# Kernel optimization log

Hardware: AMD Instinct MI355X
Metric: run time of the kernel (lower is better)

Reference implementation:

```python
import jax, jax.numpy as jnp
import numpy as np

N_NODES = 50000
N_EDGES = 800000
IN_DIM, HID_DIM, N_CLASS = 128, 128, 2
DROPOUT_P = 0.5
NEG_SLOPE = 0.01  # F.leaky_relu default


def gcn_conv(x, src, dst, W, b, n_nodes):
    """PyG GCNConv: add self-loops, sym-normalize, aggregate, then bias."""
    loops = jnp.arange(n_nodes, dtype=src.dtype)
    s = jnp.concatenate([src, loops])
    d = jnp.concatenate([dst, loops])
    # degree on A + I (edge weights = 1), counted at destination
    deg = jax.ops.segment_sum(jnp.ones_like(d, dtype=x.dtype), d, num_segments=n_nodes)
    dis = jnp.where(deg > 0, jax.lax.rsqrt(deg), 0.0)  # deg^{-1/2}
    norm = dis[s] * dis[d]                               # [E+N]
    h = x @ W                                            # [N, out]
    msg = h[s] * norm[:, None]                           # gather + scale
    out = jax.ops.segment_sum(msg, d, num_segments=n_nodes)  # scatter-add
    return out + b


def dropout(x, p, key):
    keep = 1.0 - p
    mask = jax.random.bernoulli(key, keep, x.shape)
    return jnp.where(mask, x / keep, 0.0)


def setup_inputs() -> dict:
    key = jax.random.key(0)
    ks = jax.random.split(key, 8)
    x = jax.random.normal(ks[0], (N_NODES, IN_DIM), dtype=jnp.float32)
    edge_index = jax.random.randint(ks[1], (2, N_EDGES), 0, N_NODES, dtype=jnp.int64)
    def glorot(k, fin, fout):
        lim = np.sqrt(6.0 / (fin + fout)).astype(np.float32)
        return jax.random.uniform(k, (fin, fout), jnp.float32, -lim, lim)
    W1 = glorot(ks[2], IN_DIM, HID_DIM)
    W2 = glorot(ks[3], HID_DIM, HID_DIM)
    W3 = glorot(ks[4], HID_DIM, N_CLASS)
    b1 = jnp.zeros((HID_DIM,), jnp.float32)
    b2 = jnp.zeros((HID_DIM,), jnp.float32)
    b3 = jnp.zeros((N_CLASS,), jnp.float32)
    return {"x": x, "edge_index": edge_index, "W1": W1, "b1": b1,
            "W2": W2, "b2": b2, "W3": W3, "b3": b3}


def reference(x, edge_index, W1, b1, W2, b2, W3, b3):
    src, dst = edge_index[0], edge_index[1]
    n = x.shape[0]
    dkey = jax.random.key(42)
    k1, k2 = jax.random.split(dkey)
    h = gcn_conv(x, src, dst, W1, b1, n)
    h = jax.nn.leaky_relu(h, NEG_SLOPE)
    h = dropout(h, DROPOUT_P, k1)
    h = gcn_conv(h, src, dst, W2, b2, n)
    h = jax.nn.leaky_relu(h, NEG_SLOPE)
    h = dropout(h, DROPOUT_P, k2)
    h = gcn_conv(h, src, dst, W3, b3, n)
    return jax.nn.log_softmax(h, axis=1)
```

## Files before the change

kernel.cpp:

```cpp
#include <hip/hip_runtime.h>
#include <stdint.h>

#define N_NODES 50000
#define N_EDGES 800000
#define DIM     128
#define NB   196
#define CAP  8192
#define CHUNK 2048
#define NBLK 391
#define GNODES 16
#define GGRID 3125
#define GCAP 2048
#define G3NODES 128
#define G3CAP 4096
#define ZBLK 98

typedef __attribute__((ext_vector_type(8))) unsigned short ushort8_t;
typedef __attribute__((ext_vector_type(8))) short bfrag;
typedef __attribute__((ext_vector_type(4))) float f32x4;

__host__ __device__ inline void threefry2x32(uint32_t k0, uint32_t k1,
                                             uint32_t x0, uint32_t x1,
                                             uint32_t& o0, uint32_t& o1) {
    uint32_t ks0 = k0, ks1 = k1, ks2 = k0 ^ k1 ^ 0x1BD11BDAu;
    uint32_t v0 = x0 + ks0, v1 = x1 + ks1;
#define TF_R(r) { v0 += v1; v1 = (v1 << (r)) | (v1 >> (32 - (r))); v1 ^= v0; }
    TF_R(13) TF_R(15) TF_R(26) TF_R(6)
    v0 += ks1; v1 += ks2 + 1u;
    TF_R(17) TF_R(29) TF_R(16) TF_R(24)
    v0 += ks2; v1 += ks0 + 2u;
    TF_R(13) TF_R(15) TF_R(26) TF_R(6)
    v0 += ks0; v1 += ks1 + 3u;
    TF_R(17) TF_R(29) TF_R(16) TF_R(24)
    v0 += ks1; v1 += ks2 + 4u;
    TF_R(13) TF_R(15) TF_R(26) TF_R(6)
    v0 += ks2; v1 += ks0 + 5u;
#undef TF_R
    o0 = v0; o1 = v1;
}

__device__ inline float drop_scale(uint32_t kk0, uint32_t kk1, uint32_t i) {
    uint32_t b0, b1;
    threefry2x32(kk0, kk1, 0u, i, b0, b1);
    uint32_t bits = b0 ^ b1;
    return (bits >> 31) ? 0.0f : 2.0f;
}

__device__ inline float bf2f(ushort u) {
    return __uint_as_float(((uint32_t)u) << 16);
}
__device__ inline float bfpair_lo(uint32_t u) { return __uint_as_float(u << 16); }
__device__ inline float bfpair_hi(uint32_t u) { return __uint_as_float(u & 0xffff0000u); }

__device__ inline ushort f2bf_rne(float f) {
    uint32_t bits = __float_as_uint(f);
    uint32_t lsb = (bits >> 16) & 1u;
    bits += 0x7fffu + lsb;
    return (ushort)(bits >> 16);
}

__device__ inline void acc8(float* acc, uint4 u, float d) {
    acc[0] += d * bfpair_lo(u.x); acc[1] += d * bfpair_hi(u.x);
    acc[2] += d * bfpair_lo(u.y); acc[3] += d * bfpair_hi(u.y);
    acc[4] += d * bfpair_lo(u.z); acc[5] += d * bfpair_hi(u.z);
    acc[6] += d * bfpair_lo(u.w); acc[7] += d * bfpair_hi(u.w);
}
__device__ inline void acc8p(float* acc, uint4 u) {
    acc[0] += bfpair_lo(u.x); acc[1] += bfpair_hi(u.x);
    acc[2] += bfpair_lo(u.y); acc[3] += bfpair_hi(u.y);
    acc[4] += bfpair_lo(u.z); acc[5] += bfpair_hi(u.z);
    acc[6] += bfpair_lo(u.w); acc[7] += bfpair_hi(u.w);
}

template<int F32A, int SCALE>
__device__ inline void gemm_body(const ushort* __restrict__ Xb,
                                 const float* __restrict__ Xf,
                                 const ushort* __restrict__ Wt,
                                 const float* __restrict__ dis,
                                 ushort* __restrict__ Hb, int gb, int tid) {
    int w = tid >> 6, lane = tid & 63;
    int m0 = gb * 128 + w * 32;
    int lrow = lane & 15, quad = lane >> 4;
    f32x4 acc[2][8] = {};
    for (int kt = 0; kt < DIM; kt += 32) {
        bfrag a[2], b[8];
        #pragma unroll
        for (int t = 0; t < 2; ++t) {
            int m = m0 + t * 16 + lrow;
            if (m >= N_NODES) m = 0;
            if (F32A) {
                const float* p = Xf + (size_t)m * DIM + kt + quad * 8;
                f32x4 v0 = *(const f32x4*)p;
                f32x4 v1 = *(const f32x4*)(p + 4);
                #pragma unroll
                for (int j = 0; j < 4; ++j) {
                    a[t][j]     = (short)f2bf_rne(v0[j]);
                    a[t][j + 4] = (short)f2bf_rne(v1[j]);
                }
            } else {
                a[t] = *(const bfrag*)(Xb + (size_t)m * DIM + kt + quad * 8);
            }
        }
        #pragma unroll
        for (int c = 0; c < 8; ++c) {
            int n = c * 16 + lrow;
            b[c] = *(const bfrag*)(Wt + (size_t)n * DIM + kt + quad * 8);
        }
        #pragma unroll
        for (int t = 0; t < 2; ++t)
            #pragma unroll
            for (int c = 0; c < 8; ++c)
                acc[t][c] = __builtin_amdgcn_mfma_f32_16x16x32_bf16(a[t], b[c], acc[t][c], 0, 0, 0);
    }
    #pragma unroll
    for (int t = 0; t < 2; ++t) {
        #pragma unroll
        for (int r = 0; r < 4; ++r) {
            int rowi = m0 + t * 16 + quad * 4 + r;
            if (rowi < N_NODES) {
                float dv = SCALE ? dis[rowi] : 1.0f;
                #pragma unroll
                for (int c = 0; c < 8; ++c) {
                    int feat = c * 16 + lrow;
                    float z = SCALE ? acc[t][c][r] * dv : acc[t][c][r];
                    Hb[(size_t)rowi * DIM + feat] = f2bf_rne(z);
                }
            }
        }
    }
}

__global__ __launch_bounds__(256) void k_prep(const float* __restrict__ W1,
                                              const float* __restrict__ W2,
                                              ushort* __restrict__ W1t,
                                              ushort* __restrict__ W2t,
                                              const int* __restrict__ src,
                                              const int* __restrict__ dst,
                                              uint32_t* __restrict__ gcur,
                                              uint32_t* __restrict__ packed,
                                              float* __restrict__ h3s) {
    __shared__ uint32_t h[NB];
    int b = blockIdx.x;
    int t = threadIdx.x;
    if (b < NBLK) {
        uint32_t dc[CHUNK / 256], sc[CHUNK / 256];
        if (t < NB) h[t] = 0u;
        __syncthreads();
        int base = b * CHUNK;
        #pragma unroll
        for (int i = 0; i < CHUNK / 256; ++i) {
            int e = base + i * 256 + t;
            if (e < N_EDGES) {
                dc[i] = (uint32_t)dst[e];
                sc[i] = (uint32_t)src[e];
                atomicAdd(&h[dc[i] >> 8], 1u);
            } else {
                dc[i] = 0xffffffffu;
            }
        }
        __syncthreads();
        if (t < NB) {
            uint32_t c = h[t];
            h[t] = c ? atomicAdd(&gcur[t], c) : 0u;
        }
        __syncthreads();
        #pragma unroll
        for (int i = 0; i < CHUNK / 256; ++i) {
            if (dc[i] != 0xffffffffu) {
                uint32_t d = dc[i];
                uint32_t s = sc[i];
                uint32_t bk = d >> 8;
                uint32_t pos = atomicAdd(&h[bk], 1u);
                if (pos < CAP)
                    packed[(size_t)bk * CAP + pos] = ((d & 255u) << 16) | s;
            }
        }
    } else if (b < NBLK + 128) {
        int j = (b - NBLK) * 256 + t;
        const float* W = (j < DIM * DIM) ? W1 : W2;
        ushort* Wt = (j < DIM * DIM) ? W1t : W2t;
        int i = j & (DIM * DIM - 1);
        int k = i >> 7, n = i & 127;
        Wt[n * DIM + k] = f2bf_rne(W[k * DIM + n]);
    } else {
        int idx = (b - NBLK - 128) * 256 + t;
        if (idx < (N_NODES * 2) / 4) {
            f32x4 z = {0.f, 0.f, 0.f, 0.f};
            ((f32x4*)h3s)[idx] = z;
        }
    }
}

__global__ __launch_bounds__(256) void k_fill(const uint32_t* __restrict__ gcur,
                                              const uint32_t* __restrict__ packed,
                                              uint32_t* __restrict__ row,
                                              float* __restrict__ dis,
                                              ushort* __restrict__ col16,
                                              const float* __restrict__ x,
                                              const ushort* __restrict__ W1t,
                                              ushort* __restrict__ Hb) {
    __shared__ uint32_t sdeg[256];
    __shared__ uint32_t scan[256];
    __shared__ uint32_t cur[256];
    int b = blockIdx.x;
    int t = threadIdx.x;
    if (b >= NB) {
        gemm_body<1, 0>(nullptr, x, W1t, nullptr, Hb, b - NB, t);
        return;
    }
    uint32_t n = gcur[b];
    scan[t] = (t < b) ? gcur[t] : 0u;
    __syncthreads();
    for (int off = 1; off < 256; off <<= 1) {
        uint32_t xx = (t >= off) ? scan[t - off] : 0u;
        __syncthreads();
        scan[t] += xx;
        __syncthreads();
    }
    uint32_t cbase = scan[255];
    __syncthreads();
    uint32_t pbase = (uint32_t)b * CAP;
    sdeg[t] = 0u;
    __syncthreads();
    for (uint32_t i = t; i < n; i += 256) {
        uint32_t u = packed[pbase + i];
        atomicAdd(&sdeg[u >> 16], 1u);
    }
    __syncthreads();
    uint32_t myd = sdeg[t];
    scan[t] = myd;
    __syncthreads();
    for (int off = 1; off < 256; off <<= 1) {
        uint32_t xx = (t >= off) ? scan[t - off] : 0u;
        __syncthreads();
        scan[t] += xx;
        __syncthreads();
    }
    uint32_t excl = scan[t] - myd;
    cur[t] = excl;
    int v = b * 256 + t;
    if (v <= N_NODES) row[v] = cbase + excl;
    if (v < N_NODES)  dis[v] = 1.0f / sqrtf((float)(myd + 1u));
    __syncthreads();
    for (uint32_t i = t; i < n; i += 256) {
        uint32_t u = packed[pbase + i];
        uint32_t pos = cbase + atomicAdd(&cur[u >> 16], 1u);
        col16[pos] = (ushort)(u & 0xffffu);
    }
}

template<int CLS, int SRCDIS>
__global__ __launch_bounds__(256) void k_gather_t(const uint32_t* __restrict__ row,
                                                  const ushort* __restrict__ col16,
                                                  const float* __restrict__ dis,
                                                  const ushort* __restrict__ Hb,
                                                  const float* __restrict__ bias,
                                                  ushort* __restrict__ OUTb,
                                                  const float* __restrict__ W3,
                                                  float* __restrict__ h3s,
                                                  uint32_t kk0, uint32_t kk1) {
    __shared__ ushort scol[GCAP];
    __shared__ uint32_t srow[GNODES + 1];
    int tid = threadIdx.x;
    int nbase = blockIdx.x * GNODES;
    if (tid <= GNODES) srow[tid] = row[nbase + tid];
    __syncthreads();
    uint32_t eLo = srow[0];
    uint32_t count = srow[GNODES] - eLo;
    bool staged = count <= GCAP;
    if (staged) {
        for (uint32_t i = tid; i < count; i += 256) scol[i] = col16[eLo + i];
    }
    __syncthreads();

    int nl = tid >> 4;
    int q  = tid & 15;
    int v = nbase + nl;
    float dv = dis[v];
    float acc[8];
    {
        uint4 u = *(const uint4*)(Hb + (size_t)v * DIM + q * 8);
        acc[0] = bfpair_lo(u.x); acc[1] = bfpair_hi(u.x);
        acc[2] = bfpair_lo(u.y); acc[3] = bfpair_hi(u.y);
        acc[4] = bfpair_lo(u.z); acc[5] = bfpair_hi(u.z);
        acc[6] = bfpair_lo(u.w); acc[7] = bfpair_hi(u.w);
        if (SRCDIS) {
            #pragma unroll
            for (int j = 0; j < 8; ++j) acc[j] *= dv;
        }
    }

    uint32_t e0 = srow[nl] - eLo, e1 = srow[nl + 1] - eLo;
    uint32_t e = e0;
    if (staged) {
        for (; e + 8 <= e1; e += 8) {
            uint32_t s0 = scol[e],     s1 = scol[e + 1];
            uint32_t s2 = scol[e + 2], s3 = scol[e + 3];
            uint32_t s4 = scol[e + 4], s5 = scol[e + 5];
            uint32_t s6 = scol[e + 6], s7 = scol[e + 7];
            uint4 u0 = *(const uint4*)(Hb + (size_t)s0 * DIM + q * 8);
            uint4 u1 = *(const uint4*)(Hb + (size_t)s1 * DIM + q * 8);
            uint4 u2 = *(const uint4*)(Hb + (size_t)s2 * DIM + q * 8);
            uint4 u3 = *(const uint4*)(Hb + (size_t)s3 * DIM + q * 8);
            uint4 u4 = *(const uint4*)(Hb + (size_t)s4 * DIM + q * 8);
            uint4 u5 = *(const uint4*)(Hb + (size_t)s5 * DIM + q * 8);
            uint4 u6 = *(const uint4*)(Hb + (size_t)s6 * DIM + q * 8);
            uint4 u7 = *(const uint4*)(Hb + (size_t)s7 * DIM + q * 8);
            if (SRCDIS) {
                float d0 = dis[s0], d1 = dis[s1], d2 = dis[s2], d3 = dis[s3];
                float d4 = dis[s4], d5 = dis[s5], d6 = dis[s6], d7 = dis[s7];
                acc8(acc, u0, d0); acc8(acc, u1, d1);
                acc8(acc, u2, d2); acc8(acc, u3, d3);
                acc8(acc, u4, d4); acc8(acc, u5, d5);
                acc8(acc, u6, d6); acc8(acc, u7, d7);
            } else {
                acc8p(acc, u0); acc8p(acc, u1); acc8p(acc, u2); acc8p(acc, u3);
                acc8p(acc, u4); acc8p(acc, u5); acc8p(acc, u6); acc8p(acc, u7);
            }
        }
        for (; e + 4 <= e1; e += 4) {
            uint32_t s0 = scol[e],     s1 = scol[e + 1];
            uint32_t s2 = scol[e + 2], s3 = scol[e + 3];
            uint4 u0 = *(const uint4*)(Hb + (size_t)s0 * DIM + q * 8);
            uint4 u1 = *(const uint4*)(Hb + (size_t)s1 * DIM + q * 8);
            uint4 u2 = *(const uint4*)(Hb + (size_t)s2 * DIM + q * 8);
            uint4 u3 = *(const uint4*)(Hb + (size_t)s3 * DIM + q * 8);
            if (SRCDIS) {
                float d0 = dis[s0], d1 = dis[s1], d2 = dis[s2], d3 = dis[s3];
                acc8(acc, u0, d0); acc8(acc, u1, d1);
                acc8(acc, u2, d2); acc8(acc, u3, d3);
            } else {
                acc8p(acc, u0); acc8p(acc, u1); acc8p(acc, u2); acc8p(acc, u3);
            }
        }
        for (; e < e1; ++e) {
            uint32_t s0 = scol[e];
            uint4 u0 = *(const uint4*)(Hb + (size_t)s0 * DIM + q * 8);
            if (SRCDIS) acc8(acc, u0, dis[s0]);
            else        acc8p(acc, u0);
        }
    } else {
        for (; e < e1; ++e) {
            uint32_t s0 = col16[eLo + e];
            uint4 u0 = *(const uint4*)(Hb + (size_t)s0 * DIM + q * 8);
            if (SRCDIS) acc8(acc, u0, dis[s0]);
            else        acc8p(acc, u0);
        }
    }

    int cbase = q * 8;
    uint32_t ibase = (uint32_t)(v * DIM + cbase);
    if (CLS == 0) {
        ushort8_t o;
        #pragma unroll
        for (int j = 0; j < 8; ++j) {
            float z = acc[j] * dv + bias[cbase + j];
            z = (z >= 0.f) ? z : 0.01f * z;
            z *= drop_scale(kk0, kk1, ibase + j);
            o[j] = f2bf_rne(z);
        }
        *((ushort8_t*)(OUTb + (size_t)v * DIM + cbase)) = o;
    } else {
        float o0 = 0.f, o1 = 0.f;
        #pragma unroll
        for (int j = 0; j < 8; ++j) {
            float z = acc[j] * dv + bias[cbase + j];
            z = (z >= 0.f) ? z : 0.01f * z;
            z *= drop_scale(kk0, kk1, ibase + j);
            o0 += z * W3[(cbase + j) * 2 + 0];
            o1 += z * W3[(cbase + j) * 2 + 1];
        }
        o0 += __shfl_xor(o0, 1); o0 += __shfl_xor(o0, 2);
        o0 += __shfl_xor(o0, 4); o0 += __shfl_xor(o0, 8);
        o1 += __shfl_xor(o1, 1); o1 += __shfl_xor(o1, 2);
        o1 += __shfl_xor(o1, 4); o1 += __shfl_xor(o1, 8);
        if (q == 0) {
            atomicAdd(&h3s[v * 2 + 0], o0 * dv);
            atomicAdd(&h3s[v * 2 + 1], o1 * dv);
        }
    }
}

__global__ __launch_bounds__(256) void k_gemm_bf16(const ushort* __restrict__ Xb,
                                                   const ushort* __restrict__ Wt,
                                                   const float* __restrict__ dis,
                                                   ushort* __restrict__ Hb) {
    gemm_body<0, 1>(Xb, nullptr, Wt, dis, Hb, blockIdx.x, threadIdx.x);
}

__global__ __launch_bounds__(256) void k_gather3(const uint32_t* __restrict__ row,
                                                 const ushort* __restrict__ col16,
                                                 const float* __restrict__ dis,
                                                 const float* __restrict__ H3s,
                                                 const float* __restrict__ b3,
                                                 float* __restrict__ out) {
    __shared__ ushort scol[G3CAP];
    __shared__ uint32_t srow[G3NODES + 1];
    int tid = threadIdx.x;
    int nbase = blockIdx.x * G3NODES;
    int nend = nbase + G3NODES; if (nend > N_NODES) nend = N_NODES;
    int nloc = nend - nbase;
    for (int i = tid; i <= nloc; i += 256) srow[i] = row[nbase + i];
    __syncthreads();
    uint32_t eLo = srow[0];
    uint32_t count = srow[nloc] - eLo;
    bool staged = count <= G3CAP;
    if (staged) {
        for (uint32_t i = tid; i < count; i += 256) scol[i] = col16[eLo + i];
    }
    __syncthreads();

    int nl = tid >> 1;
    int par = tid & 1;
    int v = nbase + nl;
    if (v >= N_NODES) return;
    const float2* H2 = (const float2*)H3s;
    float z0 = 0.f, z1 = 0.f;
    if (par == 0) {
        float2 h = H2[v];
        z0 = h.x; z1 = h.y;
    }
    uint32_t e0 = srow[nl] - eLo, e1 = srow[nl + 1] - eLo;
    if (staged) {
        for (uint32_t e = e0 + par; e < e1; e += 2) {
            float2 ha = H2[scol[e]];
            z0 += ha.x; z1 += ha.y;
        }
    } else {
        for (uint32_t e = e0 + par; e < e1; e += 2) {
            float2 ha = H2[col16[eLo + e]];
            z0 += ha.x; z1 += ha.y;
        }
    }
    z0 += __shfl_xor(z0, 1);
    z1 += __shfl_xor(z1, 1);
    if (par) return;
    float dv = dis[v];
    z0 = z0 * dv + b3[0];
    z1 = z1 * dv + b3[1];
    float m = fmaxf(z0, z1);
    float lse = m + logf(expf(z0 - m) + expf(z1 - m));
    out[v * 2 + 0] = z0 - lse;
    out[v * 2 + 1] = z1 - lse;
}

extern "C" void kernel_launch(void* const* d_in, const int* in_sizes, int n_in,
                              void* d_out, int out_size, void* d_ws, size_t ws_size,
                              hipStream_t stream) {
    const float* x  = (const float*)d_in[0];
    const int*   ei = (const int*)d_in[1];
    const float* W1 = (const float*)d_in[2];
    const float* b1 = (const float*)d_in[3];
    const float* W2 = (const float*)d_in[4];
    const float* b2 = (const float*)d_in[5];
    const float* W3 = (const float*)d_in[6];
    const float* b3 = (const float*)d_in[7];
    float* out = (float*)d_out;

    const int* src = ei;
    const int* dst = ei + N_EDGES;

    uint32_t* wsu = (uint32_t*)d_ws;
    float*    wsf = (float*)d_ws;
    uint32_t* gcur   = wsu;
    uint32_t* row    = wsu + 256;
    float*    dis    = wsf + 50304;
    uint32_t* packed = wsu + 100352;
    ushort*   col16  = (ushort*)(wsu + 1705984);
    ushort*   Hb     = (ushort*)(wsu + 2106112);
    ushort*   Bb     = (ushort*)(wsu + 8506112);
    ushort*   W1t    = (ushort*)(wsu + 11706112);
    ushort*   W2t    = (ushort*)(wsu + 11714304);
    float*    h3s    = wsf + 11722496;

    uint32_t k1a, k1b, k2a, k2b;
    threefry2x32(0u, 42u, 0u, 0u, k1a, k1b);
    threefry2x32(0u, 42u, 0u, 1u, k2a, k2b);

    hipMemsetAsync(gcur, 0, 256 * sizeof(uint32_t), stream);

    k_prep<<<NBLK + 128 + ZBLK, 256, 0, stream>>>(W1, W2, W1t, W2t,
                                                  src, dst, gcur, packed, h3s);

    k_fill<<<NB + 391, 256, 0, stream>>>(gcur, packed, row, dis, col16,
                                         x, W1t, Hb);

    k_gather_t<0, 1><<<GGRID, 256, 0, stream>>>(row, col16, dis, Hb, b1, Bb,
                                                nullptr, nullptr, k1a, k1b);

    k_gemm_bf16<<<(N_NODES + 127) / 128, 256, 0, stream>>>(Bb, W2t, dis, Hb);
    k_gather_t<1, 0><<<GGRID, 256, 0, stream>>>(row, col16, dis, Hb, b2, nullptr,
                                                W3, h3s, k2a, k2b);

    k_gather3<<<(N_NODES + G3NODES - 1) / G3NODES, 256, 0, stream>>>(row, col16, dis,
                                                                     h3s, b3, out);
}
```

Measured before the change: 213.9 us.

## Fuse layer-1 gather with layer-2 MFMA GEMM in one kernel

Replaces the layer-1 gather kernel and the separate bf16 GEMM kernel with one fused kernel. Each 64-node block aggregates neighbours, applies bias, leaky-relu and dropout, writes the rows to a scratch buffer, then runs MFMA over those rows against W2 and writes the dis-scaled result. This removes one kernel launch and the global round trip between kernels. In exchange the grid is much smaller (782 blocks instead of 3125), so there is less parallelism to hide gather latency. The GEMM also re-reads its rows from global memory after a block-level barrier, which relies on the block's own writes being visible to it.

```diff
diff --git a/kernel.cpp b/kernel.cpp
--- a/kernel.cpp
+++ b/kernel.cpp
@@ -11,6 +11,9 @@
 #define GNODES 16
 #define GGRID 3125
 #define GCAP 2048
+#define FN   64
+#define FBLK 782
+#define GCAP_F 3072
 #define G3NODES 128
 #define G3CAP 4096
 #define ZBLK 98
@@ -249,16 +252,148 @@
     }
 }
 
-template<int CLS, int SRCDIS>
-__global__ __launch_bounds__(256) void k_gather_t(const uint32_t* __restrict__ row,
-                                                  const ushort* __restrict__ col16,
-                                                  const float* __restrict__ dis,
-                                                  const ushort* __restrict__ Hb,
-                                                  const float* __restrict__ bias,
-                                                  ushort* __restrict__ OUTb,
-                                                  const float* __restrict__ W3,
-                                                  float* __restrict__ h3s,
-                                                  uint32_t kk0, uint32_t kk1) {
+__global__ __launch_bounds__(256) void k_fused(const uint32_t* __restrict__ row,
+                                               const ushort* __restrict__ col16,
+                                               const float* __restrict__ dis,
+                                               const ushort* __restrict__ Hb,
+                                               const float* __restrict__ bias,
+                                               ushort* __restrict__ Bs,
+                                               const ushort* __restrict__ W2t,
+                                               ushort* __restrict__ Hb2,
+                                               uint32_t kk0, uint32_t kk1) {
+    __shared__ ushort scol[GCAP_F];
+    __shared__ uint32_t srow[FN + 1];
+    int tid = threadIdx.x;
+    int nbase = blockIdx.x * FN;
+    int top = N_NODES - nbase; if (top > FN) top = FN;
+    for (int i = tid; i <= top; i += 256) srow[i] = row[nbase + i];
+    __syncthreads();
+    uint32_t eLo = srow[0];
+    uint32_t count = srow[top] - eLo;
+    bool staged = count <= GCAP_F;
+    if (staged) {
+        for (uint32_t i = tid; i < count; i += 256) scol[i] = col16[eLo + i];
+    }
+    __syncthreads();
+
+    int nl = tid >> 4;
+    int q  = tid & 15;
+    #pragma unroll
+    for (int r = 0; r < 4; ++r) {
+        int lr = r * 16 + nl;
+        int v = nbase + lr;
+        if (lr < top) {
+            float dv = dis[v];
+            float acc[8];
+            {
+                uint4 u = *(const uint4*)(Hb + (size_t)v * DIM + q * 8);
+                acc[0] = bfpair_lo(u.x); acc[1] = bfpair_hi(u.x);
+                acc[2] = bfpair_lo(u.y); acc[3] = bfpair_hi(u.y);
+                acc[4] = bfpair_lo(u.z); acc[5] = bfpair_hi(u.z);
+                acc[6] = bfpair_lo(u.w); acc[7] = bfpair_hi(u.w);
+                #pragma unroll
+                for (int j = 0; j < 8; ++j) acc[j] *= dv;
+            }
+            uint32_t e0 = srow[lr] - eLo, e1 = srow[lr + 1] - eLo;
+            uint32_t e = e0;
+            if (staged) {
+                for (; e + 8 <= e1; e += 8) {
+                    uint32_t s0 = scol[e],     s1 = scol[e + 1];
+                    uint32_t s2 = scol[e + 2], s3 = scol[e + 3];
+                    uint32_t s4 = scol[e + 4], s5 = scol[e + 5];
+                    uint32_t s6 = scol[e + 6], s7 = scol[e + 7];
+                    uint4 u0 = *(const uint4*)(Hb + (size_t)s0 * DIM + q * 8);
+                    uint4 u1 = *(const uint4*)(Hb + (size_t)s1 * DIM + q * 8);
+                    uint4 u2 = *(const uint4*)(Hb + (size_t)s2 * DIM + q * 8);
+                    uint4 u3 = *(const uint4*)(Hb + (size_t)s3 * DIM + q * 8);
+                    uint4 u4 = *(const uint4*)(Hb + (size_t)s4 * DIM + q * 8);
+                    uint4 u5 = *(const uint4*)(Hb + (size_t)s5 * DIM + q * 8);
+                    uint4 u6 = *(const uint4*)(Hb + (size_t)s6 * DIM + q * 8);
+                    uint4 u7 = *(const uint4*)(Hb + (size_t)s7 * DIM + q * 8);
+                    float d0 = dis[s0], d1 = dis[s1], d2 = dis[s2], d3 = dis[s3];
+                    float d4 = dis[s4], d5 = dis[s5], d6 = dis[s6], d7 = dis[s7];
+                    acc8(acc, u0, d0); acc8(acc, u1, d1);
+                    acc8(acc, u2, d2); acc8(acc, u3, d3);
+                    acc8(acc, u4, d4); acc8(acc, u5, d5);
+                    acc8(acc, u6, d6); acc8(acc, u7, d7);
+                }
+                for (; e + 4 <= e1; e += 4) {
+                    uint32_t s0 = scol[e],     s1 = scol[e + 1];
+                    uint32_t s2 = scol[e + 2], s3 = scol[e + 3];
+                    uint4 u0 = *(const uint4*)(Hb + (size_t)s0 * DIM + q * 8);
+                    uint4 u1 = *(const uint4*)(Hb + (size_t)s1 * DIM + q * 8);
+                    uint4 u2 = *(const uint4*)(Hb + (size_t)s2 * DIM + q * 8);
+                    uint4 u3 = *(const uint4*)(Hb + (size_t)s3 * DIM + q * 8);
+                    float d0 = dis[s0], d1 = dis[s1], d2 = dis[s2], d3 = dis[s3];
+                    acc8(acc, u0, d0); acc8(acc, u1, d1);
+                    acc8(acc, u2, d2); acc8(acc, u3, d3);
+                }
+                for (; e < e1; ++e) {
+                    uint32_t s0 = scol[e];
+                    uint4 u0 = *(const uint4*)(Hb + (size_t)s0 * DIM + q * 8);
+                    acc8(acc, u0, dis[s0]);
+                }
+            } else {
+                for (; e < e1; ++e) {
+                    uint32_t s0 = col16[eLo + e];
+                    uint4 u0 = *(const uint4*)(Hb + (size_t)s0 * DIM + q * 8);
+                    acc8(acc, u0, dis[s0]);
+                }
+            }
+            int cbase = q * 8;
+            uint32_t ibase = (uint32_t)(v * DIM + cbase);
+            ushort8_t o;
+            #pragma unroll
+            for (int j = 0; j < 8; ++j) {
+                float z = acc[j] * dv + bias[cbase + j];
+                z = (z >= 0.f) ? z : 0.01f * z;
+                z *= drop_scale(kk0, kk1, ibase + j);
+                o[j] = f2bf_rne(z);
+            }
+            *((ushort8_t*)(Bs + (size_t)v * DIM + cbase)) = o;
+        }
+    }
+    __syncthreads();
+
+    int w = tid >> 6, lane = tid & 63;
+    int lrow = lane & 15, quad = lane >> 4;
+    int m = nbase + w * 16 + lrow;
+    const ushort* Arow = Bs + (size_t)m * DIM;
+    #pragma unroll
+    for (int half = 0; half < 2; ++half) {
+        f32x4 acc[4] = {};
+        for (int kt = 0; kt < DIM; kt += 32) {
+            bfrag a = *(const bfrag*)(Arow + kt + quad * 8);
+            #pragma unroll
+            for (int c = 0; c < 4; ++c) {
+                int n = (half * 4 + c) * 16 + lrow;
+                bfrag b = *(const bfrag*)(W2t + (size_t)n * DIM + kt + quad * 8);
+                acc[c] = __builtin_amdgcn_mfma_f32_16x16x32_bf16(a, b, acc[c], 0, 0, 0);
+            }
+        }
+        #pragma unroll
+        for (int rr = 0; rr < 4; ++rr) {
+            int rowi = nbase + w * 16 + quad * 4 + rr;
+            if (rowi < N_NODES) {
+                float dvv = dis[rowi];
+                #pragma unroll
+                for (int c = 0; c < 4; ++c) {
+                    int feat = (half * 4 + c) * 16 + lrow;
+                    Hb2[(size_t)rowi * DIM + feat] = f2bf_rne(acc[c][rr] * dvv);
+                }
+            }
+        }
+    }
+}
+
+__global__ __launch_bounds__(256) void k_gather2(const uint32_t* __restrict__ row,
+                                                 const ushort* __restrict__ col16,
+                                                 const float* __restrict__ dis,
+                                                 const ushort* __restrict__ Hb,
+                                                 const float* __restrict__ bias,
+                                                 const float* __restrict__ W3,
+                                                 float* __restrict__ h3s,
+                                                 uint32_t kk0, uint32_t kk1) {
     __shared__ ushort scol[GCAP];
     __shared__ uint32_t srow[GNODES + 1];
     int tid = threadIdx.x;
@@ -284,10 +419,6 @@
         acc[2] = bfpair_lo(u.y); acc[3] = bfpair_hi(u.y);
         acc[4] = bfpair_lo(u.z); acc[5] = bfpair_hi(u.z);
         acc[6] = bfpair_lo(u.w); acc[7] = bfpair_hi(u.w);
-        if (SRCDIS) {
-            #pragma unroll
-            for (int j = 0; j < 8; ++j) acc[j] *= dv;
-        }
     }
 
     uint32_t e0 = srow[nl] - eLo, e1 = srow[nl + 1] - eLo;
@@ -306,17 +437,8 @@
             uint4 u5 = *(const uint4*)(Hb + (size_t)s5 * DIM + q * 8);
             uint4 u6 = *(const uint4*)(Hb + (size_t)s6 * DIM + q * 8);
             uint4 u7 = *(const uint4*)(Hb + (size_t)s7 * DIM + q * 8);
-            if (SRCDIS) {
-                float d0 = dis[s0], d1 = dis[s1], d2 = dis[s2], d3 = dis[s3];
-                float d4 = dis[s4], d5 = dis[s5], d6 = dis[s6], d7 = dis[s7];
-                acc8(acc, u0, d0); acc8(acc, u1, d1);
-                acc8(acc, u2, d2); acc8(acc, u3, d3);
-                acc8(acc, u4, d4); acc8(acc, u5, d5);
-                acc8(acc, u6, d6); acc8(acc, u7, d7);
-            } else {
-                acc8p(acc, u0); acc8p(acc, u1); acc8p(acc, u2); acc8p(acc, u3);
-                acc8p(acc, u4); acc8p(acc, u5); acc8p(acc, u6); acc8p(acc, u7);
-            }
+            acc8p(acc, u0); acc8p(acc, u1); acc8p(acc, u2); acc8p(acc, u3);
+            acc8p(acc, u4); acc8p(acc, u5); acc8p(acc, u6); acc8p(acc, u7);
         }
         for (; e + 4 <= e1; e += 4) {
             uint32_t s0 = scol[e],     s1 = scol[e + 1];
@@ -325,67 +447,38 @@
             uint4 u1 = *(const uint4*)(Hb + (size_t)s1 * DIM + q * 8);
             uint4 u2 = *(const uint4*)(Hb + (size_t)s2 * DIM + q * 8);
             uint4 u3 = *(const uint4*)(Hb + (size_t)s3 * DIM + q * 8);
-            if (SRCDIS) {
-                float d0 = dis[s0], d1 = dis[s1], d2 = dis[s2], d3 = dis[s3];
-                acc8(acc, u0, d0); acc8(acc, u1, d1);
-                acc8(acc, u2, d2); acc8(acc, u3, d3);
-            } else {
-                acc8p(acc, u0); acc8p(acc, u1); acc8p(acc, u2); acc8p(acc, u3);
-            }
+            acc8p(acc, u0); acc8p(acc, u1); acc8p(acc, u2); acc8p(acc, u3);
         }
         for (; e < e1; ++e) {
-            uint32_t s0 = scol[e];
-            uint4 u0 = *(const uint4*)(Hb + (size_t)s0 * DIM + q * 8);
-            if (SRCDIS) acc8(acc, u0, dis[s0]);
-            else        acc8p(acc, u0);
+            uint4 u0 = *(const uint4*)(Hb + (size_t)scol[e] * DIM + q * 8);
+            acc8p(acc, u0);
         }
     } else {
         for (; e < e1; ++e) {
-            uint32_t s0 = col16[eLo + e];
-            uint4 u0 = *(const uint4*)(Hb + (size_t)s0 * DIM + q * 8);
-            if (SRCDIS) acc8(acc, u0, dis[s0]);
-            else        acc8p(acc, u0);
+            uint4 u0 = *(const uint4*)(Hb + (size_t)col16[eLo + e] * DIM + q * 8);
+            acc8p(acc, u0);
         }
     }
 
     int cbase = q * 8;
     uint32_t ibase = (uint32_t)(v * DIM + cbase);
-    if (CLS == 0) {
-        ushort8_t o;
-        #pragma unroll
-        for (int j = 0; j < 8; ++j) {
-            float z = acc[j] * dv + bias[cbase + j];
-            z = (z >= 0.f) ? z : 0.01f * z;
-            z *= drop_scale(kk0, kk1, ibase + j);
-            o[j] = f2bf_rne(z);
-        }
-        *((ushort8_t*)(OUTb + (size_t)v * DIM + cbase)) = o;
-    } else {
-        float o0 = 0.f, o1 = 0.f;
-        #pragma unroll
-        for (int j = 0; j < 8; ++j) {
-            float z = acc[j] * dv + bias[cbase + j];
-            z = (z >= 0.f) ? z : 0.01f * z;
-            z *= drop_scale(kk0, kk1, ibase + j);
-            o0 += z * W3[(cbase + j) * 2 + 0];
-            o1 += z * W3[(cbase + j) * 2 + 1];
-        }
-        o0 += __shfl_xor(o0, 1); o0 += __shfl_xor(o0, 2);
-        o0 += __shfl_xor(o0, 4); o0 += __shfl_xor(o0, 8);
-        o1 += __shfl_xor(o1, 1); o1 += __shfl_xor(o1, 2);
-        o1 += __shfl_xor(o1, 4); o1 += __shfl_xor(o1, 8);
-        if (q == 0) {
-            atomicAdd(&h3s[v * 2 + 0], o0 * dv);
-            atomicAdd(&h3s[v * 2 + 1], o1 * dv);
-        }
-    }
-}
-
-__global__ __launch_bounds__(256) void k_gemm_bf16(const ushort* __restrict__ Xb,
-                                                   const ushort* __restrict__ Wt,
-                                                   const float* __restrict__ dis,
-                                                   ushort* __restrict__ Hb) {
-    gemm_body<0, 1>(Xb, nullptr, Wt, dis, Hb, blockIdx.x, threadIdx.x);
+    float o0 = 0.f, o1 = 0.f;
+    #pragma unroll
+    for (int j = 0; j < 8; ++j) {
+        float z = acc[j] * dv + bias[cbase + j];
+        z = (z >= 0.f) ? z : 0.01f * z;
+        z *= drop_scale(kk0, kk1, ibase + j);
+        o0 += z * W3[(cbase + j) * 2 + 0];
+        o1 += z * W3[(cbase + j) * 2 + 1];
+    }
+    o0 += __shfl_xor(o0, 1); o0 += __shfl_xor(o0, 2);
+    o0 += __shfl_xor(o0, 4); o0 += __shfl_xor(o0, 8);
+    o1 += __shfl_xor(o1, 1); o1 += __shfl_xor(o1, 2);
+    o1 += __shfl_xor(o1, 4); o1 += __shfl_xor(o1, 8);
+    if (q == 0) {
+        atomicAdd(&h3s[v * 2 + 0], o0 * dv);
+        atomicAdd(&h3s[v * 2 + 1], o1 * dv);
+    }
 }
 
 __global__ __launch_bounds__(256) void k_gather3(const uint32_t* __restrict__ row,
@@ -468,7 +561,8 @@
     uint32_t* packed = wsu + 100352;
     ushort*   col16  = (ushort*)(wsu + 1705984);
     ushort*   Hb     = (ushort*)(wsu + 2106112);
-    ushort*   Bb     = (ushort*)(wsu + 8506112);
+    ushort*   Bs     = (ushort*)(wsu + 5306112);
+    ushort*   Hb2    = (ushort*)(wsu + 8506112);
     ushort*   W1t    = (ushort*)(wsu + 11706112);
     ushort*   W2t    = (ushort*)(wsu + 11714304);
     float*    h3s    = wsf + 11722496;
@@ -485,12 +579,11 @@
     k_fill<<<NB + 391, 256, 0, stream>>>(gcur, packed, row, dis, col16,
                                          x, W1t, Hb);
 
-    k_gather_t<0, 1><<<GGRID, 256, 0, stream>>>(row, col16, dis, Hb, b1, Bb,
-                                                nullptr, nullptr, k1a, k1b);
-
-    k_gemm_bf16<<<(N_NODES + 127) / 128, 256, 0, stream>>>(Bb, W2t, dis, Hb);
-    k_gather_t<1, 0><<<GGRID, 256, 0, stream>>>(row, col16, dis, Hb, b2, nullptr,
-                                                W3, h3s, k2a, k2b);
+    k_fused<<<FBLK, 256, 0, stream>>>(row, col16, dis, Hb, b1, Bs, W2t, Hb2,
+                                      k1a, k1b);
+
+    k_gather2<<<GGRID, 256, 0, stream>>>(row, col16, dis, Hb2, b2, W3, h3s,
+                                         k2a, k2b);
 
     k_gather3<<<(N_NODES + G3NODES - 1) / G3NODES, 256, 0, stream>>>(row, col16, dis,
                                                                      h3s, b3, out);
```

Measured after the change: 212.7 us. Within noise of the previous version (-0.5%).
